# Performance work log

Hardware: AMD Instinct MI355X
Metric: run time of the kernel (lower is better)

The kernel has to match this reference:

```python
import jax, jax.numpy as jnp
import numpy as np

N_USER = 50000
N_ITEM = 100000
D = 64            # embed_size; layer_size = [64, 64, 64]
NL = 3            # number of propagation layers
NNZ = 2400000     # nonzeros of sparse Laplacian L
B = 1024          # batch of (user, pos_item, neg_item)
N = N_USER + N_ITEM


def setup_inputs() -> dict:
    key = jax.random.key(0)
    ks = jax.random.split(key, 20)
    inp = {}
    # learned parameters
    inp["user_emb"] = jax.random.normal(ks[0], (N_USER, D), jnp.float32) * 0.1
    inp["item_emb"] = jax.random.normal(ks[1], (N_ITEM, D), jnp.float32) * 0.1
    inp["lin1_w"] = jax.random.normal(ks[2], (4, D // 2), jnp.float32) * 0.5
    inp["lin1_b"] = jnp.zeros((D // 2,), jnp.float32)
    inp["lin2_w"] = jax.random.normal(ks[3], (D // 2, D), jnp.float32) * 0.2
    inp["lin2_b"] = jnp.zeros((D,), jnp.float32)
    inp["w1"] = jax.random.normal(ks[4], (NL, D, D), jnp.float32) * (1.0 / np.sqrt(D))
    inp["b1"] = jnp.zeros((NL, D), jnp.float32)
    inp["w2"] = jax.random.normal(ks[5], (NL, D, D), jnp.float32) * (1.0 / np.sqrt(D))
    inp["b2"] = jnp.zeros((NL, D), jnp.float32)
    # sparse normalized Laplacian L in COO form (eye_mat handled as +E)
    inp["lap_row"] = jax.random.randint(ks[6], (NNZ,), 0, N, jnp.int32)
    inp["lap_col"] = jax.random.randint(ks[7], (NNZ,), 0, N, jnp.int32)
    inp["lap_val"] = jax.random.uniform(ks[8], (NNZ,), jnp.float32) * (1.0 / 16.0)
    # forward args
    inp["user_idx"] = jax.random.randint(ks[9], (B,), 0, N_USER, jnp.int32)
    inp["user_feat"] = jax.random.normal(ks[10], (B, 4), jnp.float32)
    inp["pos_idx"] = jax.random.randint(ks[11], (B,), 0, N_ITEM, jnp.int32)
    inp["neg_idx"] = jax.random.randint(ks[12], (B,), 0, N_ITEM, jnp.int32)
    inp["mlp_ratio"] = jnp.float32(0.5)
    return inp


def reference(user_emb, item_emb, user_feat, lin1_w, lin1_b, lin2_w, lin2_b,
              w1, b1, w2, b2, lap_val, mlp_ratio,
              lap_row, lap_col, user_idx, pos_idx, neg_idx):
    n_user = user_emb.shape[0]
    n_nodes = user_emb.shape[0] + item_emb.shape[0]

    # user MLP: two stacked Linears (no activation in between, per Sequential)
    user_mlp = (user_feat @ lin1_w + lin1_b) @ lin2_w + lin2_b  # [B, D]
    # in-place no_grad embedding blend (stop_gradient mirrors torch.no_grad on mlp path)
    upd = user_emb[user_idx] * (1.0 - mlp_ratio) + jax.lax.stop_gradient(user_mlp) * mlp_ratio
    ue = user_emb.at[user_idx].set(upd)

    E = jnp.concatenate([ue, item_emb], axis=0)  # [N, D]

    def spmm(X):
        # L @ X via gather-multiply-segment_sum over COO nonzeros
        return jax.ops.segment_sum(lap_val[:, None] * X[lap_col], lap_row,
                                   num_segments=n_nodes)

    all_E = [E]
    for k in range(w1.shape[0]):
        L_E = spmm(E)                 # L @ E
        L_I_E = L_E + E               # (L + I) @ E
        msg = (L_I_E @ w1[k] + b1[k]) + ((L_E * E) @ w2[k] + b2[k])
        E = jax.nn.leaky_relu(msg, negative_slope=0.2)
        # F.normalize(E, p=2, dim=1) with eps=1e-12
        norm = E / jnp.maximum(jnp.linalg.norm(E, axis=1, keepdims=True), 1e-12)
        all_E.append(norm)

    all_E = jnp.concatenate(all_E, axis=1)  # [N, D*(NL+1)]
    users = all_E[:n_user]
    items = all_E[n_user:]
    return (users[user_idx], items[pos_idx], items[neg_idx])
```

## Files before the change

kernel.cpp:

```cpp
#include <hip/hip_runtime.h>
#include <hip/hip_bf16.h>

#define N_USERC 50000
#define N_ITEMC 100000
#define NNODE   150000
#define DIM     64
#define NLAYERS 3
#define NNZC    2400000
#define BATCH   1024

#define RPB     128
#define NBUCK   1172
#define NCHUNK  512
#define CHUNK   4688
#define CAPB    3072
#define NPARTB  8

using short8 = __attribute__((ext_vector_type(8))) short;
using us8    = __attribute__((ext_vector_type(8))) unsigned short;
using f32x4  = __attribute__((ext_vector_type(4))) float;
using uintx4 = __attribute__((ext_vector_type(4))) unsigned;

__device__ __forceinline__ float bf2f(ushort u) {
    return __uint_as_float(((unsigned)u) << 16);
}
__device__ __forceinline__ ushort f2bf(float f) {
    unsigned u = __float_as_uint(f);
    u += 0x7FFF + ((u >> 16) & 1);
    return (ushort)(u >> 16);
}

__device__ __forceinline__ int block_excl_scan(int v, int* lds) {
    int lane = threadIdx.x & 63;
    int wid  = threadIdx.x >> 6;
    int nw   = (blockDim.x + 63) >> 6;
    int inc = v;
#pragma unroll
    for (int o = 1; o < 64; o <<= 1) {
        int n = __shfl_up(inc, o, 64);
        if (lane >= o) inc += n;
    }
    if (lane == 63) lds[wid] = inc;
    __syncthreads();
    if (wid == 0) {
        int tv = (lane < nw) ? lds[lane] : 0;
#pragma unroll
        for (int o = 1; o < 16; o <<= 1) {
            int n = __shfl_up(tv, o, 64);
            if (lane >= o) tv += n;
        }
        if (lane < nw) lds[lane] = tv;
    }
    __syncthreads();
    int woff = (wid == 0) ? 0 : lds[wid - 1];
    return woff + (inc - v);
}

__global__ __launch_bounds__(256) void k_prep(const float* __restrict__ ue,
                                              const float* __restrict__ ie,
                                              ushort* __restrict__ Ebf,
                                              const float* __restrict__ w1,
                                              const float* __restrict__ w2,
                                              ushort* __restrict__ Wtg,
                                              const int* __restrict__ user_idx,
                                              int* __restrict__ winner) {
    int i = blockIdx.x * blockDim.x + threadIdx.x;
    const int userEnd = N_USERC * DIM / 4;
    const int total   = NNODE * DIM / 4;
    if (i < total) {
        float4 v;
        if (i < userEnd) v = ((const float4*)ue)[i];
        else             v = ((const float4*)ie)[i - userEnd];
        ushort4 b;
        b.x = f2bf(v.x); b.y = f2bf(v.y); b.z = f2bf(v.z); b.w = f2bf(v.w);
        ((ushort4*)Ebf)[i] = b;
    }
    if (i < NLAYERS * 64 * 128) {
        int layer = i >> 13;
        int rem = i & 8191;
        int n = rem >> 7, kk = rem & 127;
        float v = (kk < 64) ? w1[layer * 4096 + kk * 64 + n]
                            : w2[layer * 4096 + (kk - 64) * 64 + n];
        Wtg[i] = f2bf(v);
    }
    if (i < BATCH) atomicMax(&winner[user_idx[i]], i);
}

__global__ void k_mlp_update(const float* __restrict__ user_emb,
                             const float* __restrict__ user_feat,
                             const float* __restrict__ l1w, const float* __restrict__ l1b,
                             const float* __restrict__ l2w, const float* __restrict__ l2b,
                             const float* __restrict__ ratio_p,
                             const int* __restrict__ user_idx,
                             const int* __restrict__ winner,
                             ushort* __restrict__ Ebf) {
    int b = blockIdx.x;
    int d = threadIdx.x;
    int u = user_idx[b];
    if (winner[u] != b) return;
    float ratio = ratio_p[0];
    float uf0 = user_feat[b * 4 + 0], uf1 = user_feat[b * 4 + 1];
    float uf2 = user_feat[b * 4 + 2], uf3 = user_feat[b * 4 + 3];
    float acc = l2b[d];
#pragma unroll
    for (int j = 0; j < 32; ++j) {
        float h = l1b[j] + uf0 * l1w[0 * 32 + j] + uf1 * l1w[1 * 32 + j]
                         + uf2 * l1w[2 * 32 + j] + uf3 * l1w[3 * 32 + j];
        acc += h * l2w[j * DIM + d];
    }
    float v = user_emb[u * DIM + d] * (1.f - ratio) + acc * ratio;
    Ebf[u * DIM + d] = f2bf(v);
}

__global__ __launch_bounds__(256) void k_chunksort(const int* __restrict__ rows,
                                                   const int* __restrict__ cols,
                                                   const float* __restrict__ vals,
                                                   unsigned long long* __restrict__ tmp,
                                                   ushort* __restrict__ scanT,
                                                   int* __restrict__ winner) {
    __shared__ int hist[NBUCK];
    __shared__ int sutil[16];
    __shared__ unsigned long long stag[CHUNK];

    const int c = blockIdx.x;
    const int s = c * CHUNK;
    const int e = (s + CHUNK < NNZC) ? s + CHUNK : NNZC;
    const int t = threadIdx.x;

    for (int i = c * 256 + t; i < N_USERC; i += NCHUNK * 256) winner[i] = -1;

    for (int i = t; i < NBUCK; i += 256) hist[i] = 0;
    __syncthreads();
    for (int i = s + t; i < e; i += 256) atomicAdd(&hist[rows[i] >> 7], 1);
    __syncthreads();

    int loc[5];
    int sum = 0;
#pragma unroll
    for (int k = 0; k < 5; ++k) {
        int idx = t * 5 + k;
        int v = (idx < NBUCK) ? hist[idx] : 0;
        loc[k] = sum;
        sum += v;
    }
    int excl = block_excl_scan(sum, sutil);
#pragma unroll
    for (int k = 0; k < 5; ++k) {
        int idx = t * 5 + k;
        if (idx < NBUCK) hist[idx] = excl + loc[k];
    }
    __syncthreads();

    for (int i = t; i < NBUCK; i += 256) scanT[(size_t)i * NCHUNK + c] = (ushort)hist[i];
    if (t == 0) scanT[(size_t)NBUCK * NCHUNK + c] = (ushort)(e - s);
    __syncthreads();

    for (int i = s + t; i < e; i += 256) {
        int r = rows[i];
        int b = r >> 7, ro = r & 127;
        unsigned hi = ((unsigned)ro << 18) | (unsigned)cols[i];
        unsigned long long pk = ((unsigned long long)hi << 32) | (unsigned)__float_as_uint(vals[i]);
        int pos = atomicAdd(&hist[b], 1);
        stag[pos] = pk;
    }
    __syncthreads();

    int n = e - s;
    for (int i = t; i < n; i += 256) tmp[s + i] = stag[i];
}

__global__ __launch_bounds__(256) void k_buckcnt(const ushort* __restrict__ scanT,
                                                 int* __restrict__ bstart,
                                                 int* __restrict__ rowptr) {
    int wid  = threadIdx.x >> 6;
    int lane = threadIdx.x & 63;
    int b = blockIdx.x * 4 + wid;
    if (blockIdx.x == 0 && threadIdx.x == 0) {
        bstart[NBUCK] = NNZC;
        rowptr[NNODE] = NNZC;
    }
    if (b >= NBUCK) return;
    us8 v = *(const us8*)&scanT[(size_t)b * NCHUNK + lane * 8];
    int ss = (int)v[0] + (int)v[1] + (int)v[2] + (int)v[3]
           + (int)v[4] + (int)v[5] + (int)v[6] + (int)v[7];
#pragma unroll
    for (int m = 32; m; m >>= 1) ss += __shfl_xor(ss, m, 64);
    if (lane == 0) bstart[b] = ss;
}

__global__ __launch_bounds__(256) void k_compact(const ushort* __restrict__ scanT,
                                                 const int* __restrict__ bstart,
                                                 const unsigned long long* __restrict__ tmp,
                                                 unsigned long long* __restrict__ csr,
                                                 int* __restrict__ rowptr) {
    __shared__ int runstart[NCHUNK];
    __shared__ int pref[NCHUNK + 1];
    __shared__ int sutil[16];
    __shared__ int rcur[RPB];
    __shared__ unsigned long long stag[CAPB];
    const int b = blockIdx.x;
    const int t = threadIdx.x;

    for (int r = t; r < NCHUNK; r += 256) {
        int s0 = scanT[(size_t)b * NCHUNK + r];
        int s1 = scanT[(size_t)(b + 1) * NCHUNK + r];
        runstart[r] = r * CHUNK + s0;
        pref[r] = s1 - s0;
    }
    if (t < RPB) rcur[t] = 0;
    __syncthreads();
    int v0 = pref[t * 2], v1 = pref[t * 2 + 1];
    int sum = v0 + v1;
    int excl = block_excl_scan(sum, sutil);
    pref[t * 2] = excl;
    pref[t * 2 + 1] = excl + v0;
    if (t == 255) pref[NCHUNK] = excl + sum;
    __syncthreads();

    const int total = pref[NCHUNK];
    const int obase = bstart[b];

    if (total <= CAPB) {
        for (int r = t; r < NCHUNK; r += 256) {
            int p0 = pref[r], p1 = pref[r + 1];
            int rs = runstart[r];
            for (int i = p0; i < p1; ++i) stag[i] = tmp[rs + (i - p0)];
        }
        __syncthreads();
        for (int i = t; i < total; i += 256)
            atomicAdd(&rcur[(int)(stag[i] >> 50) & 127], 1);
        __syncthreads();
        int rv = (t < RPB) ? rcur[t] : 0;
        int rex = block_excl_scan(rv, sutil);
        if (t < RPB) {
            rcur[t] = rex;
            int grow = b * RPB + t;
            if (grow < NNODE) rowptr[grow] = obase + rex;
        }
        __syncthreads();
        for (int i = t; i < total; i += 256) {
            unsigned long long pk = stag[i];
            int ro = (int)(pk >> 50) & 127;
            int pos = atomicAdd(&rcur[ro], 1);
            csr[obase + pos] = pk;
        }
        return;
    }

    for (int i = t; i < total; i += 256) {
        int lo = 0, hi = NCHUNK - 1;
        while (lo < hi) {
            int mid = (lo + hi + 1) >> 1;
            if (pref[mid] <= i) lo = mid; else hi = mid - 1;
        }
        unsigned long long pk = tmp[runstart[lo] + (i - pref[lo])];
        atomicAdd(&rcur[(int)(pk >> 50) & 127], 1);
    }
    __syncthreads();
    int rv = (t < RPB) ? rcur[t] : 0;
    int rex = block_excl_scan(rv, sutil);
    if (t < RPB) {
        rcur[t] = rex;
        int grow = b * RPB + t;
        if (grow < NNODE) rowptr[grow] = obase + rex;
    }
    __syncthreads();
    for (int i = t; i < total; i += 256) {
        int lo = 0, hi = NCHUNK - 1;
        while (lo < hi) {
            int mid = (lo + hi + 1) >> 1;
            if (pref[mid] <= i) lo = mid; else hi = mid - 1;
        }
        unsigned long long pk = tmp[runstart[lo] + (i - pref[lo])];
        int ro = (int)(pk >> 50) & 127;
        int pos = atomicAdd(&rcur[ro], 1);
        csr[obase + pos] = pk;
    }
}

__global__ __launch_bounds__(256) void k_spmm(const int* __restrict__ rowptr,
                                              const unsigned long long* __restrict__ csr,
                                              const ushort* __restrict__ Ebf,
                                              ushort* __restrict__ Abf) {
    int lane = threadIdx.x & 63;
    int row  = blockIdx.x * 4 + (threadIdx.x >> 6);
    row = __builtin_amdgcn_readfirstlane(row);
    if (row >= NNODE) return;
    int s = __builtin_amdgcn_readfirstlane(rowptr[row]);
    int e = __builtin_amdgcn_readfirstlane(rowptr[row + 1]);
    const ushort* Ep = Ebf + lane;
    float eo = bf2f(Ebf[row * DIM + lane]);
    float acc = 0.f;
    int j = s;
    for (; j + 16 <= e; j += 16) {
        unsigned long long pk[16];
        float ev[16];
#pragma unroll
        for (int k = 0; k < 16; ++k) pk[k] = csr[j + k];
#pragma unroll
        for (int k = 0; k < 16; ++k) {
            int col = (int)(pk[k] >> 32) & 0x3FFFF;
            ev[k] = bf2f(Ep[col * DIM]);
        }
#pragma unroll
        for (int k = 0; k < 16; ++k)
            acc += __uint_as_float((unsigned)pk[k]) * ev[k];
    }
    if (j < e) {
        int m = e - j;
        unsigned long long pk[16];
        float ev[16];
#pragma unroll
        for (int k = 0; k < 16; ++k) pk[k] = csr[j + k];
#pragma unroll
        for (int k = 0; k < 16; ++k) {
            int col = (k < m) ? ((int)(pk[k] >> 32) & 0x3FFFF) : 0;
            ev[k] = bf2f(Ep[col * DIM]);
        }
#pragma unroll
        for (int k = 0; k < 16; ++k) {
            unsigned v = (k < m) ? (unsigned)pk[k] : 0u;
            acc += __uint_as_float(v) * ev[k];
        }
    }
    __builtin_nontemporal_store(f2bf(acc + eo), &Abf[row * 128 + lane]);
    __builtin_nontemporal_store(f2bf(acc * eo), &Abf[row * 128 + 64 + lane]);
}

__global__ __launch_bounds__(256) void k_transform(const ushort* __restrict__ Abf,
                                                   const ushort* __restrict__ Wtg,
                                                   const float* __restrict__ b1k,
                                                   const float* __restrict__ b2k,
                                                   ushort* __restrict__ Ebf_out) {
    __shared__ ushort A_s[64 * 136];
    __shared__ ushort W_s[64 * 136];
    __shared__ float  bias_s[64];

    const int t = threadIdx.x;
    const int rowbase = blockIdx.x * 64;
    if (t < 64) bias_s[t] = b1k[t] + b2k[t];

#pragma unroll
    for (int it = 0; it < 4; ++it) {
        int task = t + 256 * it;
        int n = task >> 4, k = (task & 15) * 8;
        uint4 wv = *(const uint4*)&Wtg[n * 128 + k];
        *(uint4*)&W_s[n * 136 + k] = wv;
    }
#pragma unroll
    for (int it = 0; it < 4; ++it) {
        int task = t + 256 * it;
        int rl = task >> 4, k8 = (task & 15) * 8;
        int row = rowbase + rl;
        uintx4 v = {0u, 0u, 0u, 0u};
        if (row < NNODE)
            v = __builtin_nontemporal_load((const uintx4*)&Abf[row * 128 + k8]);
        *(uintx4*)&A_s[rl * 136 + k8] = v;
    }
    __syncthreads();

    const int w = t >> 6, l = t & 63;
    const int m16 = l & 15;
    const int q   = l >> 4;
    const int lm  = w * 16 + m16;

    f32x4 z = {0.f, 0.f, 0.f, 0.f};
    f32x4 acc[4] = {z, z, z, z};
#pragma unroll
    for (int ks = 0; ks < 4; ++ks) {
        short8 af = *(const short8*)&A_s[lm * 136 + ks * 32 + q * 8];
#pragma unroll
        for (int nt = 0; nt < 4; ++nt) {
            short8 wf = *(const short8*)&W_s[(nt * 16 + m16) * 136 + ks * 32 + q * 8];
            acc[nt] = __builtin_amdgcn_mfma_f32_16x16x32_bf16(af, wf, acc[nt], 0, 0, 0);
        }
    }
    __syncthreads();

    float* Cs = (float*)A_s;
#pragma unroll
    for (int nt = 0; nt < 4; ++nt) {
        int col = nt * 16 + m16;
#pragma unroll
        for (int r = 0; r < 4; ++r) {
            int lrow = w * 16 + q * 4 + r;
            Cs[lrow * 68 + col] = acc[nt][r];
        }
    }
    __syncthreads();

#pragma unroll
    for (int it = 0; it < 2; ++it) {
        int task = t + 256 * it;
        int rl = task >> 3, col = (task & 7) * 8;
        int row = rowbase + rl;
        if (row < NNODE) {
            float4 v0 = *(const float4*)&Cs[rl * 68 + col];
            float4 v1 = *(const float4*)&Cs[rl * 68 + col + 4];
            float o[8] = {v0.x, v0.y, v0.z, v0.w, v1.x, v1.y, v1.z, v1.w};
            ushort ob[8];
#pragma unroll
            for (int j = 0; j < 8; ++j) {
                float v = o[j] + bias_s[col + j];
                v = v >= 0.f ? v : 0.2f * v;
                ob[j] = f2bf(v);
            }
            uint4 pb;
            pb.x = (unsigned)ob[0] | ((unsigned)ob[1] << 16);
            pb.y = (unsigned)ob[2] | ((unsigned)ob[3] << 16);
            pb.z = (unsigned)ob[4] | ((unsigned)ob[5] << 16);
            pb.w = (unsigned)ob[6] | ((unsigned)ob[7] << 16);
            *(uint4*)&Ebf_out[row * 64 + col] = pb;
        }
    }
}

__global__ __launch_bounds__(256) void k_gather(const ushort* __restrict__ Ebf,
                                                const int* __restrict__ user_idx,
                                                const int* __restrict__ pos_idx,
                                                const int* __restrict__ neg_idx,
                                                float* __restrict__ out,
                                                int seg, int normalize) {
    int wid  = threadIdx.x >> 6;
    int lane = threadIdx.x & 63;
    int o = blockIdx.x * 4 + wid;
    if (o >= 3 * BATCH) return;
    int g = o >> 10, b = o & 1023;
    int row;
    if (g == 0)      row = user_idx[b];
    else if (g == 1) row = N_USERC + pos_idx[b];
    else             row = N_USERC + neg_idx[b];
    float v = bf2f(Ebf[row * DIM + lane]);
    if (normalize) {
        float ss = v * v;
#pragma unroll
        for (int m = 32; m; m >>= 1) ss += __shfl_xor(ss, m, 64);
        float nrm = sqrtf(ss);
        nrm = fmaxf(nrm, 1e-12f);
        v = v / nrm;
    }
    out[(g * BATCH + b) * 256 + seg * 64 + lane] = v;
}

extern "C" void kernel_launch(void* const* d_in, const int* in_sizes, int n_in,
                              void* d_out, int out_size, void* d_ws, size_t ws_size,
                              hipStream_t stream) {
    const float* user_emb  = (const float*)d_in[0];
    const float* item_emb  = (const float*)d_in[1];
    const float* lin1_w    = (const float*)d_in[2];
    const float* lin1_b    = (const float*)d_in[3];
    const float* lin2_w    = (const float*)d_in[4];
    const float* lin2_b    = (const float*)d_in[5];
    const float* w1        = (const float*)d_in[6];
    const float* b1        = (const float*)d_in[7];
    const float* w2        = (const float*)d_in[8];
    const float* b2        = (const float*)d_in[9];
    const int*   lap_row   = (const int*)d_in[10];
    const int*   lap_col   = (const int*)d_in[11];
    const float* lap_val   = (const float*)d_in[12];
    const int*   user_idx  = (const int*)d_in[13];
    const float* user_feat = (const float*)d_in[14];
    const int*   pos_idx   = (const int*)d_in[15];
    const int*   neg_idx   = (const int*)d_in[16];
    const float* mlp_ratio = (const float*)d_in[17];
    float* out = (float*)d_out;

    size_t off = 0;
    auto carve = [&](size_t bytes) { size_t r = off; off = (off + bytes + 255) & ~(size_t)255; return r; };
    size_t oL      = carve((size_t)NNODE * DIM * 4);
    size_t oEbf    = carve((size_t)NNODE * DIM * 2);
    size_t oCsr    = carve((size_t)NNZC * 8);
    size_t oScan   = carve((size_t)NCHUNK * (NBUCK + 1) * 2);
    size_t oBcnt   = carve((size_t)NBUCK * 4);
    size_t oBstart = carve((size_t)(NBUCK + 1) * 4);
    size_t oRowptr = carve((size_t)(NNODE + 1) * 4);
    size_t oWinner = carve((size_t)N_USERC * 4);
    size_t oBcntP  = carve((size_t)NPARTB * NBUCK * 4);
    (void)ws_size; (void)oBcnt; (void)oBcntP;

    char* base = (char*)d_ws;
    ushort*             Abf    = (ushort*)(base + oL);
    unsigned long long* tmp    = (unsigned long long*)(base + oL);
    ushort*             Ebf    = (ushort*)(base + oEbf);
    unsigned long long* csr    = (unsigned long long*)(base + oCsr);
    ushort*             scanT  = (ushort*)(base + oScan);
    int*                bstart = (int*)(base + oBstart);
    int*                rowptr = (int*)(base + oRowptr);
    int*                winner = (int*)(base + oWinner);
    ushort*             Wtg    = (ushort*)(base + oScan);

    k_chunksort<<<NCHUNK, 256, 0, stream>>>(lap_row, lap_col, lap_val, tmp, scanT, winner);
    k_buckcnt<<<(NBUCK + 3) / 4, 256, 0, stream>>>(scanT, bstart, rowptr);
    k_compact<<<NBUCK, 256, 0, stream>>>(scanT, bstart, tmp, csr, rowptr);

    k_prep<<<(NNODE * DIM / 4 + 255) / 256, 256, 0, stream>>>(
        user_emb, item_emb, Ebf, w1, w2, Wtg, user_idx, winner);
    k_mlp_update<<<BATCH, 64, 0, stream>>>(user_emb, user_feat, lin1_w, lin1_b,
                                           lin2_w, lin2_b, mlp_ratio, user_idx, winner, Ebf);
    k_gather<<<(3 * BATCH) / 4, 256, 0, stream>>>(Ebf, user_idx, pos_idx, neg_idx, out, 0, 0);

    for (int k = 0; k < NLAYERS; ++k) {
        k_spmm<<<(NNODE + 3) / 4, 256, 0, stream>>>(rowptr, csr, Ebf, Abf);
        k_transform<<<(NNODE + 63) / 64, 256, 0, stream>>>(
            Abf, Wtg + (size_t)k * 64 * 128, b1 + (size_t)k * DIM,
            b2 + (size_t)k * DIM, Ebf);
        k_gather<<<(3 * BATCH) / 4, 256, 0, stream>>>(Ebf, user_idx, pos_idx, neg_idx,
                                                      out, k + 1, 1);
    }
}
```

Before: 417.1 us.

## Fold small kernels into neighbours to cut launch count

Removes the bucket-count kernel by computing each bucket's output base inside the compact kernel with a block scan over the scan table. The winner atomicMax moves into compact block 0, and the MLP blend is folded into the bf16 conversion in prep. The per-layer gather of the previous layer's embeddings is appended as extra blocks to the next spmm launch, leaving only a final gather. This drops about six kernel launches and their serialization gaps. In exchange it adds redundant scans per compact block and per-thread MLP recomputation in prep.

```diff
diff --git a/kernel.cpp b/kernel.cpp
--- a/kernel.cpp
+++ b/kernel.cpp
@@ -15,9 +15,10 @@
 #define CHUNK   4688
 #define CAPB    3072
 #define NPARTB  8
+#define NROWB   37500
+#define NGATHB  768
 
 using short8 = __attribute__((ext_vector_type(8))) short;
-using us8    = __attribute__((ext_vector_type(8))) unsigned short;
 using f32x4  = __attribute__((ext_vector_type(4))) float;
 using uintx4 = __attribute__((ext_vector_type(4))) unsigned;
 
@@ -62,18 +63,51 @@
                                               const float* __restrict__ w1,
                                               const float* __restrict__ w2,
                                               ushort* __restrict__ Wtg,
-                                              const int* __restrict__ user_idx,
-                                              int* __restrict__ winner) {
+                                              const float* __restrict__ user_feat,
+                                              const float* __restrict__ l1w,
+                                              const float* __restrict__ l1b,
+                                              const float* __restrict__ l2w,
+                                              const float* __restrict__ l2b,
+                                              const float* __restrict__ ratio_p,
+                                              const int* __restrict__ winner,
+                                              int* __restrict__ rowptr) {
     int i = blockIdx.x * blockDim.x + threadIdx.x;
     const int userEnd = N_USERC * DIM / 4;
     const int total   = NNODE * DIM / 4;
+    if (i == 0) rowptr[NNODE] = NNZC;
     if (i < total) {
         float4 v;
         if (i < userEnd) v = ((const float4*)ue)[i];
         else             v = ((const float4*)ie)[i - userEnd];
-        ushort4 b;
-        b.x = f2bf(v.x); b.y = f2bf(v.y); b.z = f2bf(v.z); b.w = f2bf(v.w);
-        ((ushort4*)Ebf)[i] = b;
+        if (i < userEnd) {
+            int u = i >> 4;
+            int b = winner[u];
+            if (b >= 0) {
+                int d0 = (i & 15) * 4;
+                float ratio = ratio_p[0];
+                float uf0 = user_feat[b * 4 + 0], uf1 = user_feat[b * 4 + 1];
+                float uf2 = user_feat[b * 4 + 2], uf3 = user_feat[b * 4 + 3];
+                float a0 = l2b[d0 + 0], a1 = l2b[d0 + 1];
+                float a2 = l2b[d0 + 2], a3 = l2b[d0 + 3];
+#pragma unroll
+                for (int j = 0; j < 32; ++j) {
+                    float h = l1b[j] + uf0 * l1w[0 * 32 + j] + uf1 * l1w[1 * 32 + j]
+                                     + uf2 * l1w[2 * 32 + j] + uf3 * l1w[3 * 32 + j];
+                    a0 += h * l2w[j * DIM + d0 + 0];
+                    a1 += h * l2w[j * DIM + d0 + 1];
+                    a2 += h * l2w[j * DIM + d0 + 2];
+                    a3 += h * l2w[j * DIM + d0 + 3];
+                }
+                float om = 1.f - ratio;
+                v.x = v.x * om + a0 * ratio;
+                v.y = v.y * om + a1 * ratio;
+                v.z = v.z * om + a2 * ratio;
+                v.w = v.w * om + a3 * ratio;
+            }
+        }
+        ushort4 b4;
+        b4.x = f2bf(v.x); b4.y = f2bf(v.y); b4.z = f2bf(v.z); b4.w = f2bf(v.w);
+        ((ushort4*)Ebf)[i] = b4;
     }
     if (i < NLAYERS * 64 * 128) {
         int layer = i >> 13;
@@ -83,33 +117,6 @@
                             : w2[layer * 4096 + (kk - 64) * 64 + n];
         Wtg[i] = f2bf(v);
     }
-    if (i < BATCH) atomicMax(&winner[user_idx[i]], i);
-}
-
-__global__ void k_mlp_update(const float* __restrict__ user_emb,
-                             const float* __restrict__ user_feat,
-                             const float* __restrict__ l1w, const float* __restrict__ l1b,
-                             const float* __restrict__ l2w, const float* __restrict__ l2b,
-                             const float* __restrict__ ratio_p,
-                             const int* __restrict__ user_idx,
-                             const int* __restrict__ winner,
-                             ushort* __restrict__ Ebf) {
-    int b = blockIdx.x;
-    int d = threadIdx.x;
-    int u = user_idx[b];
-    if (winner[u] != b) return;
-    float ratio = ratio_p[0];
-    float uf0 = user_feat[b * 4 + 0], uf1 = user_feat[b * 4 + 1];
-    float uf2 = user_feat[b * 4 + 2], uf3 = user_feat[b * 4 + 3];
-    float acc = l2b[d];
-#pragma unroll
-    for (int j = 0; j < 32; ++j) {
-        float h = l1b[j] + uf0 * l1w[0 * 32 + j] + uf1 * l1w[1 * 32 + j]
-                         + uf2 * l1w[2 * 32 + j] + uf3 * l1w[3 * 32 + j];
-        acc += h * l2w[j * DIM + d];
-    }
-    float v = user_emb[u * DIM + d] * (1.f - ratio) + acc * ratio;
-    Ebf[u * DIM + d] = f2bf(v);
 }
 
 __global__ __launch_bounds__(256) void k_chunksort(const int* __restrict__ rows,
@@ -169,46 +176,46 @@
     for (int i = t; i < n; i += 256) tmp[s + i] = stag[i];
 }
 
-__global__ __launch_bounds__(256) void k_buckcnt(const ushort* __restrict__ scanT,
-                                                 int* __restrict__ bstart,
-                                                 int* __restrict__ rowptr) {
-    int wid  = threadIdx.x >> 6;
-    int lane = threadIdx.x & 63;
-    int b = blockIdx.x * 4 + wid;
-    if (blockIdx.x == 0 && threadIdx.x == 0) {
-        bstart[NBUCK] = NNZC;
-        rowptr[NNODE] = NNZC;
-    }
-    if (b >= NBUCK) return;
-    us8 v = *(const us8*)&scanT[(size_t)b * NCHUNK + lane * 8];
-    int ss = (int)v[0] + (int)v[1] + (int)v[2] + (int)v[3]
-           + (int)v[4] + (int)v[5] + (int)v[6] + (int)v[7];
-#pragma unroll
-    for (int m = 32; m; m >>= 1) ss += __shfl_xor(ss, m, 64);
-    if (lane == 0) bstart[b] = ss;
-}
-
 __global__ __launch_bounds__(256) void k_compact(const ushort* __restrict__ scanT,
-                                                 const int* __restrict__ bstart,
                                                  const unsigned long long* __restrict__ tmp,
                                                  unsigned long long* __restrict__ csr,
-                                                 int* __restrict__ rowptr) {
+                                                 int* __restrict__ rowptr,
+                                                 const int* __restrict__ user_idx,
+                                                 int* __restrict__ winner) {
     __shared__ int runstart[NCHUNK];
     __shared__ int pref[NCHUNK + 1];
     __shared__ int sutil[16];
     __shared__ int rcur[RPB];
+    __shared__ int obase_s;
     __shared__ unsigned long long stag[CAPB];
     const int b = blockIdx.x;
     const int t = threadIdx.x;
 
-    for (int r = t; r < NCHUNK; r += 256) {
-        int s0 = scanT[(size_t)b * NCHUNK + r];
-        int s1 = scanT[(size_t)(b + 1) * NCHUNK + r];
-        runstart[r] = r * CHUNK + s0;
-        pref[r] = s1 - s0;
+    if (b == 0) {
+        for (int i = t; i < BATCH; i += 256) atomicMax(&winner[user_idx[i]], i);
+    }
+
+    int s0v0, s0v1;
+    {
+        int r0 = t, r1 = t + 256;
+        int a0 = scanT[(size_t)b * NCHUNK + r0];
+        int a1 = scanT[(size_t)(b + 1) * NCHUNK + r0];
+        int c0 = scanT[(size_t)b * NCHUNK + r1];
+        int c1 = scanT[(size_t)(b + 1) * NCHUNK + r1];
+        runstart[r0] = r0 * CHUNK + a0;
+        runstart[r1] = r1 * CHUNK + c0;
+        pref[r0] = a1 - a0;
+        pref[r1] = c1 - c0;
+        s0v0 = a0; s0v1 = c0;
     }
     if (t < RPB) rcur[t] = 0;
     __syncthreads();
+
+    {
+        int msum = s0v0 + s0v1;
+        int mex = block_excl_scan(msum, sutil);
+        if (t == 255) obase_s = mex + msum;
+    }
     int v0 = pref[t * 2], v1 = pref[t * 2 + 1];
     int sum = v0 + v1;
     int excl = block_excl_scan(sum, sutil);
@@ -218,7 +225,7 @@
     __syncthreads();
 
     const int total = pref[NCHUNK];
-    const int obase = bstart[b];
+    const int obase = obase_s;
 
     if (total <= CAPB) {
         for (int r = t; r < NCHUNK; r += 256) {
@@ -281,11 +288,37 @@
 __global__ __launch_bounds__(256) void k_spmm(const int* __restrict__ rowptr,
                                               const unsigned long long* __restrict__ csr,
                                               const ushort* __restrict__ Ebf,
-                                              ushort* __restrict__ Abf) {
+                                              ushort* __restrict__ Abf,
+                                              const int* __restrict__ user_idx,
+                                              const int* __restrict__ pos_idx,
+                                              const int* __restrict__ neg_idx,
+                                              float* __restrict__ out,
+                                              int seg, int normalize) {
     int lane = threadIdx.x & 63;
-    int row  = blockIdx.x * 4 + (threadIdx.x >> 6);
+    int wid  = threadIdx.x >> 6;
+
+    if (blockIdx.x >= NROWB) {
+        int o = (blockIdx.x - NROWB) * 4 + wid;
+        int g = o >> 10, b = o & 1023;
+        int row;
+        if (g == 0)      row = user_idx[b];
+        else if (g == 1) row = N_USERC + pos_idx[b];
+        else             row = N_USERC + neg_idx[b];
+        float v = bf2f(Ebf[row * DIM + lane]);
+        if (normalize) {
+            float ss = v * v;
+#pragma unroll
+            for (int m = 32; m; m >>= 1) ss += __shfl_xor(ss, m, 64);
+            float nrm = sqrtf(ss);
+            nrm = fmaxf(nrm, 1e-12f);
+            v = v / nrm;
+        }
+        out[(g * BATCH + b) * 256 + seg * 64 + lane] = v;
+        return;
+    }
+
+    int row = blockIdx.x * 4 + wid;
     row = __builtin_amdgcn_readfirstlane(row);
-    if (row >= NNODE) return;
     int s = __builtin_amdgcn_readfirstlane(rowptr[row]);
     int e = __builtin_amdgcn_readfirstlane(rowptr[row + 1]);
     const ushort* Ep = Ebf + lane;
@@ -476,7 +509,7 @@
     size_t oRowptr = carve((size_t)(NNODE + 1) * 4);
     size_t oWinner = carve((size_t)N_USERC * 4);
     size_t oBcntP  = carve((size_t)NPARTB * NBUCK * 4);
-    (void)ws_size; (void)oBcnt; (void)oBcntP;
+    (void)ws_size; (void)oBcnt; (void)oBstart; (void)oBcntP;
 
     char* base = (char*)d_ws;
     ushort*             Abf    = (ushort*)(base + oL);
@@ -484,27 +517,24 @@
     ushort*             Ebf    = (ushort*)(base + oEbf);
     unsigned long long* csr    = (unsigned long long*)(base + oCsr);
     ushort*             scanT  = (ushort*)(base + oScan);
-    int*                bstart = (int*)(base + oBstart);
     int*                rowptr = (int*)(base + oRowptr);
     int*                winner = (int*)(base + oWinner);
     ushort*             Wtg    = (ushort*)(base + oScan);
 
     k_chunksort<<<NCHUNK, 256, 0, stream>>>(lap_row, lap_col, lap_val, tmp, scanT, winner);
-    k_buckcnt<<<(NBUCK + 3) / 4, 256, 0, stream>>>(scanT, bstart, rowptr);
-    k_compact<<<NBUCK, 256, 0, stream>>>(scanT, bstart, tmp, csr, rowptr);
+    k_compact<<<NBUCK, 256, 0, stream>>>(scanT, tmp, csr, rowptr, user_idx, winner);
 
     k_prep<<<(NNODE * DIM / 4 + 255) / 256, 256, 0, stream>>>(
-        user_emb, item_emb, Ebf, w1, w2, Wtg, user_idx, winner);
-    k_mlp_update<<<BATCH, 64, 0, stream>>>(user_emb, user_feat, lin1_w, lin1_b,
-                                           lin2_w, lin2_b, mlp_ratio, user_idx, winner, Ebf);
-    k_gather<<<(3 * BATCH) / 4, 256, 0, stream>>>(Ebf, user_idx, pos_idx, neg_idx, out, 0, 0);
+        user_emb, item_emb, Ebf, w1, w2, Wtg,
+        user_feat, lin1_w, lin1_b, lin2_w, lin2_b, mlp_ratio, winner, rowptr);
 
     for (int k = 0; k < NLAYERS; ++k) {
-        k_spmm<<<(NNODE + 3) / 4, 256, 0, stream>>>(rowptr, csr, Ebf, Abf);
+        k_spmm<<<NROWB + NGATHB, 256, 0, stream>>>(rowptr, csr, Ebf, Abf,
+                                                   user_idx, pos_idx, neg_idx, out,
+                                                   k, k > 0 ? 1 : 0);
         k_transform<<<(NNODE + 63) / 64, 256, 0, stream>>>(
             Abf, Wtg + (size_t)k * 64 * 128, b1 + (size_t)k * DIM,
             b2 + (size_t)k * DIM, Ebf);
-        k_gather<<<(3 * BATCH) / 4, 256, 0, stream>>>(Ebf, user_idx, pos_idx, neg_idx,
-                                                      out, k + 1, 1);
-    }
-}
+    }
+    k_gather<<<NGATHB, 256, 0, stream>>>(Ebf, user_idx, pos_idx, neg_idx, out, NLAYERS, 1);
+}
```

Result: no change. 420.2 us (+0.7%).
